# Performance work log

Measured on AMD Instinct MI355X. Metric: run time of the kernel, lower is better.

Reference implementation:

```python
import jax, jax.numpy as jnp
import numpy as np
import math

B = 262144
STATE = 6
TOTAL_MEAS = 27
HID = 256
INPUT_DIM = TOTAL_MEAS * 2 + 1 + STATE + 12  # 73
PI = math.pi
NORM_R_SCALE = 500.0 / 150000.0
ANG_IDX = np.array([0, 1, 3, 4, 6, 9, 10, 12, 13, 15, 18, 19, 21, 22, 24])
ANG_MASK = np.zeros((TOTAL_MEAS,), dtype=bool)
ANG_MASK[ANG_IDX] = True


def setup_inputs() -> dict:
    key = jax.random.key(0)
    ks = jax.random.split(key, 16)
    s = lambda fan: 1.0 / math.sqrt(fan)
    inp = {
        "meas": jax.random.normal(ks[0], (B, TOTAL_MEAS), jnp.float32),
        "mask": jnp.ones((B, TOTAL_MEAS), jnp.float32),
        "dt": jax.random.uniform(ks[1], (B,), jnp.float32),
        "baselines": jax.random.normal(ks[2], (B, 12), jnp.float32),
        "x_prev": jax.random.normal(ks[3], (B, STATE), jnp.float32),
        "hx": jnp.zeros((B, HID), jnp.float32),
        # GRU params (torch gate order: r, z, n)
        "W_ih": jax.random.uniform(ks[4], (3 * HID, INPUT_DIM), jnp.float32, -s(HID), s(HID)),
        "W_hh": jax.random.uniform(ks[5], (3 * HID, HID), jnp.float32, -s(HID), s(HID)),
        "b_ih": jax.random.uniform(ks[6], (3 * HID,), jnp.float32, -s(HID), s(HID)),
        "b_hh": jax.random.uniform(ks[7], (3 * HID,), jnp.float32, -s(HID), s(HID)),
        # LayerNorm
        "ln_g": jnp.ones((HID,), jnp.float32),
        "ln_b": jnp.zeros((HID,), jnp.float32),
        # MLP head: 256 -> 256 -> 128 -> 6*27
        "W1": jax.random.uniform(ks[8], (256, HID), jnp.float32, -s(HID), s(HID)),
        "b1": jax.random.uniform(ks[9], (256,), jnp.float32, -s(HID), s(HID)),
        "W2": jax.random.uniform(ks[10], (128, 256), jnp.float32, -s(256), s(256)),
        "b2": jax.random.uniform(ks[11], (128,), jnp.float32, -s(256), s(256)),
        "W3": jax.random.uniform(ks[12], (STATE * TOTAL_MEAS, 128), jnp.float32, -s(128), s(128)),
        "b3": jax.random.uniform(ks[13], (STATE * TOTAL_MEAS,), jnp.float32, -s(128), s(128)),
    }
    return inp


def _wrap_angle(a):
    two_pi = 2.0 * PI
    return a - two_pi * jnp.round(a / two_pi)


def _platform_y_pred(x_rel):
    # x_rel: [B, 6] -> [B, 9] radar/EO measurement
    r_xy = jnp.sqrt(x_rel[:, 0] ** 2 + x_rel[:, 2] ** 2 + 1e-9)
    az = jnp.arctan2(x_rel[:, 2], x_rel[:, 0]) / PI
    el = jnp.arctan2(x_rel[:, 4], r_xy) / PI
    r = jnp.sqrt(x_rel[:, 0] ** 2 + x_rel[:, 2] ** 2 + x_rel[:, 4] ** 2 + 1e-9)
    z = jnp.zeros_like(r)
    return jnp.stack([az, el, r, az, el, z, az, z, z], axis=1)


def _forward(meas, mask, dt, baselines, x_prev, hx,
             W_ih, W_hh, b_ih, b_hh, ln_g, ln_b, W1, b1, W2, b2, W3, b3):
    # f_predict (CV model): x0 += dt*x1, x2 += dt*x3, x4 += dt*x5
    dt_scaled = dt * NORM_R_SCALE  # [B]
    zcol = jnp.zeros_like(x_prev[:, :1])
    shift = jnp.concatenate([x_prev[:, 1:2], zcol, x_prev[:, 3:4], zcol, x_prev[:, 5:6], zcol], axis=1)
    x_minus = x_prev + dt_scaled[:, None] * shift  # [B, 6]

    y_pred = jnp.concatenate([
        _platform_y_pred(x_minus),
        _platform_y_pred(x_minus - baselines[:, 0:6]),
        _platform_y_pred(x_minus - baselines[:, 6:12]),
    ], axis=1)  # [B, 27]

    innov = meas - y_pred
    wrapped = _wrap_angle(innov * PI) / PI
    innov = jnp.where(jnp.asarray(ANG_MASK)[None, :], wrapped, innov)
    innov = innov * mask

    rnn_in = jnp.concatenate([innov, mask, dt[:, None], x_minus, baselines], axis=1)  # [B, 73]

    # single-step GRU (torch semantics, gate order r,z,n)
    gi = rnn_in @ W_ih.T + b_ih  # [B, 3H]
    gh = hx @ W_hh.T + b_hh      # [B, 3H]
    gi_r, gi_z, gi_n = jnp.split(gi, 3, axis=1)
    gh_r, gh_z, gh_n = jnp.split(gh, 3, axis=1)
    r = jax.nn.sigmoid(gi_r + gh_r)
    z = jax.nn.sigmoid(gi_z + gh_z)
    n = jnp.tanh(gi_n + r * gh_n)
    h_new = (1.0 - z) * n + z * hx  # [B, H]

    # LayerNorm
    mu = jnp.mean(h_new, axis=-1, keepdims=True)
    var = jnp.var(h_new, axis=-1, keepdims=True)
    h_ln = (h_new - mu) / jnp.sqrt(var + 1e-5) * ln_g + ln_b

    # MLP gain head (dropout inactive at inference)
    f1 = jax.nn.relu(h_ln @ W1.T + b1)
    f2 = jax.nn.relu(f1 @ W2.T + b2)
    K = (f2 @ W3.T + b3).reshape(-1, STATE, TOTAL_MEAS)
    K = jnp.clip(K, -3.0, 3.0)

    correction = jnp.einsum('bsm,bm->bs', K, innov)
    x_new = jnp.clip(x_minus + correction, -5.0, 5.0)
    return x_new, h_new


def reference(meas, mask, dt, baselines, x_prev, hx,
              W_ih, W_hh, b_ih, b_hh, ln_g, ln_b, W1, b1, W2, b2, W3, b3):
    return _forward(meas, mask, dt, baselines, x_prev, hx,
                    W_ih, W_hh, b_ih, b_hh, ln_g, ln_b, W1, b1, W2, b2, W3, b3)
```

## Files before the change

kernel.cpp:

```cpp
#include <hip/hip_runtime.h>
#include <math.h>

#define B_TOTAL  262144
#define ROWS     64
#define NWG      (B_TOTAL/ROWS)
#define NTHR     512
#define PI_F     3.14159265358979323846f
#define NORM_R   (500.0f/150000.0f)

typedef float  f32x4  __attribute__((ext_vector_type(4)));
typedef short  bf16x8 __attribute__((ext_vector_type(8)));

#define SRZ 352
#define SNI 96
#define SNH 256
#define SW1 256
#define SW2 256
#define SW3 128
#define OFF_RZ 0
#define OFF_NI (OFF_RZ + 512*SRZ)
#define OFF_NH (OFF_NI + 256*SNI)
#define OFF_W1 (OFF_NH + 256*SNH)
#define OFF_W2 (OFF_W1 + 256*SW1)
#define OFF_W3 (OFF_W2 + 128*SW2)
#define W_TOTAL (OFF_W3 + 256*SW3)

#define RSTRIDE 104
#define LDS_HB   (ROWS*RSTRIDE*2)
#define LDS_F1   (LDS_HB + ROWS*256*2)
#define LDS_STG  (LDS_F1 + ROWS*256*2)
#define LDS_XMC  (LDS_STG + 2*16384)
#define LDS_TOTAL (LDS_XMC + ROWS*6*4)

#define WAIT_VM2 asm volatile("s_waitcnt vmcnt(2)" ::: "memory")
#define WAIT_VM0 asm volatile("s_waitcnt vmcnt(0)" ::: "memory")
#define BARv     __builtin_amdgcn_s_barrier()

__device__ __forceinline__ ushort f2bf(float f){
    union { float f; unsigned u; } v; v.f = f;
    unsigned r = v.u + 0x7FFFu + ((v.u >> 16) & 1u);
    return (ushort)(r >> 16);
}
__device__ __forceinline__ float b2f(ushort u){
    union { unsigned u; float f; } v; v.u = ((unsigned)u) << 16;
    return v.f;
}
__device__ __forceinline__ float sigm(float x){ return 1.0f/(1.0f+__expf(-x)); }
__device__ __forceinline__ float tanh_(float x){ return 1.0f - 2.0f/(__expf(2.0f*x)+1.0f); }
__device__ __forceinline__ int swzb(int row, int k){
    return ((row<<9) + (k<<1)) ^ ((row&7)<<4);
}

__device__ __forceinline__ void stageA(const ushort* pb, int stride, int koff,
                                       char* dst, int w, int lane) {
    #pragma unroll
    for (int i = 0; i < 2; ++i) {
        int idx  = (w*2 + i)*64 + lane;
        int col  = idx >> 2;
        int kq   = (idx & 3) ^ ((col >> 1) & 3);
        const ushort* g = pb + (size_t)col*stride + koff + kq*8;
        __builtin_amdgcn_global_load_lds(
            (const __attribute__((address_space(1))) void*)g,
            (__attribute__((address_space(3))) void*)(dst + (w*2+i)*1024),
            16, 0, 0);
    }
}
__device__ __forceinline__ void stageB(const ushort* pb, int stride, int koff,
                                       char* dst, int w, int lane) {
    #pragma unroll
    for (int i = 0; i < 2; ++i) {
        int idx  = (w*2 + i)*64 + lane;
        int col  = idx >> 3;
        int kq   = (idx & 7) ^ (col & 7);
        const ushort* g = pb + (size_t)col*stride + koff + kq*8;
        __builtin_amdgcn_global_load_lds(
            (const __attribute__((address_space(1))) void*)g,
            (__attribute__((address_space(3))) void*)(dst + (w*2+i)*1024),
            16, 0, 0);
    }
}
__device__ __forceinline__ bf16x8 rdA16(const char* sb, int col, int lk){
    int slot = lk ^ ((col >> 1) & 3);
    return *(const bf16x8*)(sb + col*64 + slot*16);
}
__device__ __forceinline__ bf16x8 rdB16(const char* sb, int col, int ksub, int lk){
    int slot = ((ksub<<2)|lk) ^ (col & 7);
    return *(const bf16x8*)(sb + col*128 + slot*16);
}

__global__ void prep_weights(const float* __restrict__ W_ih, const float* __restrict__ W_hh,
                             const float* __restrict__ W1, const float* __restrict__ W2,
                             const float* __restrict__ W3, ushort* __restrict__ ws)
{
    int id = blockIdx.x*256 + threadIdx.x;
    if (id >= W_TOTAL) return;
    float v = 0.0f;
    if (id < OFF_NI) {
        int t = id; int n = t / SRZ, k = t - n*SRZ;
        if (k < 73) v = W_ih[n*73 + k];
        else if (k >= 96) v = W_hh[n*256 + (k-96)];
    } else if (id < OFF_NH) {
        int t = id - OFF_NI; int n = t / SNI, k = t - n*SNI;
        if (k < 73) v = W_ih[(512+n)*73 + k];
    } else if (id < OFF_W1) {
        int t = id - OFF_NH; int n = t >> 8, k = t & 255;
        v = W_hh[(512+n)*256 + k];
    } else if (id < OFF_W2) {
        int t = id - OFF_W1; int n = t >> 8, k = t & 255;
        v = W1[n*256 + k];
    } else if (id < OFF_W3) {
        int t = id - OFF_W2; int n = t >> 8, k = t & 255;
        v = W2[n*256 + k];
    } else {
        int t = id - OFF_W3; int n = t >> 7, k = t & 127;
        if (n < 162) v = W3[n*128 + k];
    }
    ws[id] = f2bf(v);
}

__global__ __launch_bounds__(NTHR, 2) void knet_mfma(
    const float* __restrict__ meas, const float* __restrict__ mask,
    const float* __restrict__ dt,   const float* __restrict__ baselines,
    const float* __restrict__ x_prev, const float* __restrict__ hx,
    const float* __restrict__ b_ih, const float* __restrict__ b_hh,
    const float* __restrict__ ln_g, const float* __restrict__ ln_b,
    const float* __restrict__ b1,   const float* __restrict__ b2,
    const float* __restrict__ b3,
    const ushort* __restrict__ ws,
    float* __restrict__ out)
{
    extern __shared__ char smem[];
    ushort* Rb  = (ushort*)smem;
    char*   Hb  = smem + LDS_HB;
    char*   F1  = smem + LDS_F1;
    char*   STG = smem + LDS_STG;
    float*  xmc = (float*)(smem + LDS_XMC);

    const int tid  = threadIdx.x;
    const int w    = __builtin_amdgcn_readfirstlane(tid >> 6);
    const int nq   = w & 3;
    const int mh   = w >> 2;
    const int lane = tid & 63;
    const int lr   = lane & 15;
    const int lk   = lane >> 4;
    const int lk8  = lk * 8;
    const int row0 = blockIdx.x * ROWS;
    const int mrow = mh*32 + lr;
    float* hout = out + (size_t)B_TOTAL*6;

    stageA(ws + OFF_RZ, SRZ, 0, STG, w, lane);

    {
        const int part = w;
        const int row  = lane;
        const int gb   = row0 + row;
        if (part < 4) {
            const float dtv = dt[gb];
            const float dts = dtv * NORM_R;
            float xp[6], xm[6];
            #pragma unroll
            for (int s = 0; s < 6; ++s) xp[s] = x_prev[(size_t)gb*6 + s];
            xm[0] = xp[0] + dts*xp[1]; xm[1] = xp[1];
            xm[2] = xp[2] + dts*xp[3]; xm[3] = xp[3];
            xm[4] = xp[4] + dts*xp[5]; xm[5] = xp[5];
            if (part < 3) {
                float xr[6];
                #pragma unroll
                for (int s = 0; s < 6; ++s) {
                    float b = (part == 0) ? 0.0f : baselines[(size_t)gb*12 + (part-1)*6 + s];
                    xr[s] = xm[s] - b;
                }
                float rxy = sqrtf(xr[0]*xr[0] + xr[2]*xr[2] + 1e-9f);
                float azv = atan2f(xr[2], xr[0]) * (1.0f/PI_F);
                float elv = atan2f(xr[4], rxy)   * (1.0f/PI_F);
                float rrv = sqrtf(xr[0]*xr[0] + xr[2]*xr[2] + xr[4]*xr[4] + 1e-9f);
                float y[9] = {azv, elv, rrv, azv, elv, 0.0f, azv, 0.0f, 0.0f};
                const bool ang[9] = {true,true,false,true,true,false,true,false,false};
                #pragma unroll
                for (int i = 0; i < 9; ++i) {
                    int m = part*9 + i;
                    float ms = mask[(size_t)gb*27 + m];
                    float v  = meas[(size_t)gb*27 + m] - y[i];
                    if (ang[i]) v = v - 2.0f*rintf(v*0.5f);
                    v *= ms;
                    Rb[row*RSTRIDE + m]      = f2bf(v);
                    Rb[row*RSTRIDE + 27 + m] = f2bf(ms);
                }
            } else {
                Rb[row*RSTRIDE + 54] = f2bf(dtv);
                #pragma unroll
                for (int s = 0; s < 6; ++s) Rb[row*RSTRIDE + 55 + s] = f2bf(xm[s]);
                #pragma unroll
                for (int q = 0; q < 12; ++q) Rb[row*RSTRIDE + 61 + q] = f2bf(baselines[(size_t)gb*12 + q]);
                #pragma unroll
                for (int k = 73; k < 96; ++k) Rb[row*RSTRIDE + k] = 0;
                #pragma unroll
                for (int s = 0; s < 6; ++s) xmc[row*6 + s] = xm[s];
            }
        }
        const size_t hbase = (size_t)row0 * 256;
        #pragma unroll
        for (int ii = 0; ii < 4; ++ii) {
            int cid = tid + ii*NTHR;
            int r  = cid >> 5;
            int k0 = (cid & 31) << 3;
            const float4* p = (const float4*)(hx + hbase + (size_t)r*256 + k0);
            float4 u = p[0], v2 = p[1];
            bf16x8 o;
            o[0]=(short)f2bf(u.x);  o[1]=(short)f2bf(u.y);  o[2]=(short)f2bf(u.z);  o[3]=(short)f2bf(u.w);
            o[4]=(short)f2bf(v2.x); o[5]=(short)f2bf(v2.y); o[6]=(short)f2bf(v2.z); o[7]=(short)f2bf(v2.w);
            *(bf16x8*)(Hb + swzb(r, k0)) = o;
        }
    }
    __syncthreads();

    f32x4 ar[2][4], az_[2][4], gi[2][4], gh[2][4];
    #pragma unroll
    for (int i = 0; i < 2; ++i)
        #pragma unroll
        for (int j = 0; j < 4; ++j) {
            ar[i][j]=(f32x4){0,0,0,0}; az_[i][j]=(f32x4){0,0,0,0};
            gi[i][j]=(f32x4){0,0,0,0}; gh[i][j]=(f32x4){0,0,0,0};
        }

    for (int kb = 0; kb < 11; ++kb) {
        char* nb = STG + (((kb+1)&1)<<14);
        if (kb < 10) stageA(ws + OFF_RZ, SRZ, (kb+1)*32, nb, w, lane);
        else         stageA(ws + OFF_RZ + (size_t)256*SRZ, SRZ, 0, nb, w, lane);
        WAIT_VM2; BARv;
        char* sb = STG + ((kb&1)<<14);
        bf16x8 a0, a1;
        if (kb < 3) { a0 = *(const bf16x8*)(Rb + mrow*RSTRIDE + kb*32 + lk8);
                      a1 = *(const bf16x8*)(Rb + (mrow+16)*RSTRIDE + kb*32 + lk8); }
        else        { a0 = *(const bf16x8*)(Hb + swzb(mrow,    (kb-3)*32 + lk8));
                      a1 = *(const bf16x8*)(Hb + swzb(mrow+16, (kb-3)*32 + lk8)); }
        __builtin_amdgcn_s_setprio(1);
        #pragma unroll
        for (int j = 0; j < 4; ++j) {
            bf16x8 b = rdA16(sb, nq*64 + j*16 + lr, lk);
            ar[0][j] = __builtin_amdgcn_mfma_f32_16x16x32_bf16(a0, b, ar[0][j], 0,0,0);
            ar[1][j] = __builtin_amdgcn_mfma_f32_16x16x32_bf16(a1, b, ar[1][j], 0,0,0);
        }
        __builtin_amdgcn_s_setprio(0);
        BARv;
    }
    for (int kb = 0; kb < 11; ++kb) {
        char* nb = STG + (((kb)&1)<<14);
        if (kb < 10) stageA(ws + OFF_RZ + (size_t)256*SRZ, SRZ, (kb+1)*32, nb, w, lane);
        else         stageA(ws + OFF_NI, SNI, 0, nb, w, lane);
        WAIT_VM2; BARv;
        char* sb = STG + (((kb+1)&1)<<14);
        bf16x8 a0, a1;
        if (kb < 3) { a0 = *(const bf16x8*)(Rb + mrow*RSTRIDE + kb*32 + lk8);
                      a1 = *(const bf16x8*)(Rb + (mrow+16)*RSTRIDE + kb*32 + lk8); }
        else        { a0 = *(const bf16x8*)(Hb + swzb(mrow,    (kb-3)*32 + lk8));
                      a1 = *(const bf16x8*)(Hb + swzb(mrow+16, (kb-3)*32 + lk8)); }
        __builtin_amdgcn_s_setprio(1);
        #pragma unroll
        for (int j = 0; j < 4; ++j) {
            bf16x8 b = rdA16(sb, nq*64 + j*16 + lr, lk);
            az_[0][j] = __builtin_amdgcn_mfma_f32_16x16x32_bf16(a0, b, az_[0][j], 0,0,0);
            az_[1][j] = __builtin_amdgcn_mfma_f32_16x16x32_bf16(a1, b, az_[1][j], 0,0,0);
        }
        __builtin_amdgcn_s_setprio(0);
        BARv;
    }
    for (int s = 0; s < 11; ++s) {
        char* nb = STG + (((s+23)&1)<<14);
        if (s < 2)       stageA(ws + OFF_NI, SNI, (s+1)*32, nb, w, lane);
        else if (s < 10) stageA(ws + OFF_NH, SNH, (s-2)*32, nb, w, lane);
        else             stageA(ws + OFF_W1, SW1, 0,        nb, w, lane);
        WAIT_VM2; BARv;
        char* sb = STG + (((s+22)&1)<<14);
        bf16x8 a0, a1;
        if (s < 3) { a0 = *(const bf16x8*)(Rb + mrow*RSTRIDE + s*32 + lk8);
                     a1 = *(const bf16x8*)(Rb + (mrow+16)*RSTRIDE + s*32 + lk8); }
        else       { a0 = *(const bf16x8*)(Hb + swzb(mrow,    (s-3)*32 + lk8));
                     a1 = *(const bf16x8*)(Hb + swzb(mrow+16, (s-3)*32 + lk8)); }
        __builtin_amdgcn_s_setprio(1);
        if (s < 3) {
            #pragma unroll
            for (int j = 0; j < 4; ++j) {
                bf16x8 b = rdA16(sb, nq*64 + j*16 + lr, lk);
                gi[0][j] = __builtin_amdgcn_mfma_f32_16x16x32_bf16(a0, b, gi[0][j], 0,0,0);
                gi[1][j] = __builtin_amdgcn_mfma_f32_16x16x32_bf16(a1, b, gi[1][j], 0,0,0);
            }
        } else {
            #pragma unroll
            for (int j = 0; j < 4; ++j) {
                bf16x8 b = rdA16(sb, nq*64 + j*16 + lr, lk);
                gh[0][j] = __builtin_amdgcn_mfma_f32_16x16x32_bf16(a0, b, gh[0][j], 0,0,0);
                gh[1][j] = __builtin_amdgcn_mfma_f32_16x16x32_bf16(a1, b, gh[1][j], 0,0,0);
            }
        }
        __builtin_amdgcn_s_setprio(0);
        BARv;
    }
    #pragma unroll
    for (int j = 0; j < 4; ++j) {
        int c = nq*64 + j*16 + lr;
        float brv = b_ih[c] + b_hh[c];
        float bzv = b_ih[256+c] + b_hh[256+c];
        float binv = b_ih[512+c], bhnv = b_hh[512+c];
        #pragma unroll
        for (int i = 0; i < 2; ++i)
            #pragma unroll
            for (int e = 0; e < 4; ++e) {
                int row = mh*32 + i*16 + lk*4 + e;
                float rg = sigm(ar[i][j][e] + brv);
                float zg = sigm(az_[i][j][e] + bzv);
                float ng = tanh_(gi[i][j][e] + binv + rg*(gh[i][j][e] + bhnv));
                float hxv = b2f(*(const ushort*)(Hb + swzb(row, c)));
                float hn = (1.0f - zg)*ng + zg*hxv;
                *(ushort*)(F1 + swzb(row, c)) = f2bf(hn);
            }
    }
    __syncthreads();

    {
        const int row = tid >> 3;
        const int o   = tid & 7;
        bf16x8 ch[4];
        float sum = 0.0f, sq = 0.0f;
        #pragma unroll
        for (int c4 = 0; c4 < 4; ++c4) {
            ch[c4] = *(const bf16x8*)(F1 + swzb(row, o*32 + c4*8));
            #pragma unroll
            for (int e = 0; e < 8; ++e) {
                float f = b2f((ushort)ch[c4][e]);
                sum += f; sq += f*f;
            }
        }
        sum += __shfl_xor(sum, 1); sum += __shfl_xor(sum, 2); sum += __shfl_xor(sum, 4);
        sq  += __shfl_xor(sq, 1);  sq  += __shfl_xor(sq, 2);  sq  += __shfl_xor(sq, 4);
        float mu   = sum * (1.0f/256.0f);
        float rstd = rsqrtf(sq*(1.0f/256.0f) - mu*mu + 1e-5f);
        #pragma unroll
        for (int c4 = 0; c4 < 4; ++c4) {
            int col0 = o*32 + c4*8;
            float4 g0 = *(const float4*)(ln_g + col0), g1 = *(const float4*)(ln_g + col0 + 4);
            float4 bb0 = *(const float4*)(ln_b + col0), bb1 = *(const float4*)(ln_b + col0 + 4);
            bf16x8 oo;
            oo[0] = (short)f2bf((b2f((ushort)ch[c4][0]) - mu)*rstd*g0.x + bb0.x);
            oo[1] = (short)f2bf((b2f((ushort)ch[c4][1]) - mu)*rstd*g0.y + bb0.y);
            oo[2] = (short)f2bf((b2f((ushort)ch[c4][2]) - mu)*rstd*g0.z + bb0.z);
            oo[3] = (short)f2bf((b2f((ushort)ch[c4][3]) - mu)*rstd*g0.w + bb0.w);
            oo[4] = (short)f2bf((b2f((ushort)ch[c4][4]) - mu)*rstd*g1.x + bb1.x);
            oo[5] = (short)f2bf((b2f((ushort)ch[c4][5]) - mu)*rstd*g1.y + bb1.y);
            oo[6] = (short)f2bf((b2f((ushort)ch[c4][6]) - mu)*rstd*g1.z + bb1.z);
            oo[7] = (short)f2bf((b2f((ushort)ch[c4][7]) - mu)*rstd*g1.w + bb1.w);
            *(bf16x8*)(Hb + swzb(row, col0)) = oo;
        }
        #pragma unroll
        for (int i = 0; i < 8; ++i) {
            int chunk = i*NTHR + tid;
            int r2 = chunk >> 6;
            int c16 = chunk & 63;
            uint2 d = *(const uint2*)(F1 + swzb(r2, c16*4));
            float4 o4;
            o4.x = b2f((ushort)(d.x & 0xffffu)); o4.y = b2f((ushort)(d.x >> 16));
            o4.z = b2f((ushort)(d.y & 0xffffu)); o4.w = b2f((ushort)(d.y >> 16));
            *(float4*)(hout + (size_t)(row0+r2)*256 + c16*4) = o4;
        }
    }
    __syncthreads();

    {
        f32x4 c2[2][4];
        #pragma unroll
        for (int i = 0; i < 2; ++i)
            #pragma unroll
            for (int j = 0; j < 4; ++j) c2[i][j] = (f32x4){0,0,0,0};
        for (int kb = 0; kb < 8; ++kb) {
            char* nb = STG + (((kb+34)&1)<<14);
            if (kb < 7) stageA(ws + OFF_W1, SW1, (kb+1)*32, nb, w, lane);
            else        stageB(ws + OFF_W2, SW2, 0,         nb, w, lane);
            WAIT_VM2; BARv;
            char* sb = STG + (((kb+33)&1)<<14);
            bf16x8 a0 = *(const bf16x8*)(Hb + swzb(mrow,    kb*32 + lk8));
            bf16x8 a1 = *(const bf16x8*)(Hb + swzb(mrow+16, kb*32 + lk8));
            __builtin_amdgcn_s_setprio(1);
            #pragma unroll
            for (int j = 0; j < 4; ++j) {
                bf16x8 b = rdA16(sb, nq*64 + j*16 + lr, lk);
                c2[0][j] = __builtin_amdgcn_mfma_f32_16x16x32_bf16(a0, b, c2[0][j], 0,0,0);
                c2[1][j] = __builtin_amdgcn_mfma_f32_16x16x32_bf16(a1, b, c2[1][j], 0,0,0);
            }
            __builtin_amdgcn_s_setprio(0);
            BARv;
        }
        #pragma unroll
        for (int j = 0; j < 4; ++j) {
            int c = nq*64 + j*16 + lr;
            float bv = b1[c];
            #pragma unroll
            for (int i = 0; i < 2; ++i)
                #pragma unroll
                for (int e = 0; e < 4; ++e) {
                    int row = mh*32 + i*16 + lk*4 + e;
                    *(ushort*)(F1 + swzb(row, c)) = f2bf(fmaxf(c2[i][j][e] + bv, 0.0f));
                }
        }
    }
    __syncthreads();

    ushort* F2 = (ushort*)Hb;
    {
        f32x4 c3[2][2];
        #pragma unroll
        for (int i = 0; i < 2; ++i)
            #pragma unroll
            for (int j = 0; j < 2; ++j) c3[i][j] = (f32x4){0,0,0,0};
        for (int kb = 0; kb < 4; ++kb) {
            char* nb = STG + (((kb+42)&1)<<14);
            if (kb < 3) stageB(ws + OFF_W2, SW2, (kb+1)*64, nb, w, lane);
            else        stageA(ws + OFF_W3, SW3, 0,         nb, w, lane);
            WAIT_VM2; BARv;
            char* sb = STG + (((kb+41)&1)<<14);
            __builtin_amdgcn_s_setprio(1);
            #pragma unroll
            for (int ksub = 0; ksub < 2; ++ksub) {
                bf16x8 a0 = *(const bf16x8*)(F1 + swzb(mrow,    kb*64 + ksub*32 + lk8));
                bf16x8 a1 = *(const bf16x8*)(F1 + swzb(mrow+16, kb*64 + ksub*32 + lk8));
                #pragma unroll
                for (int j = 0; j < 2; ++j) {
                    bf16x8 b = rdB16(sb, nq*32 + j*16 + lr, ksub, lk);
                    c3[0][j] = __builtin_amdgcn_mfma_f32_16x16x32_bf16(a0, b, c3[0][j], 0,0,0);
                    c3[1][j] = __builtin_amdgcn_mfma_f32_16x16x32_bf16(a1, b, c3[1][j], 0,0,0);
                }
            }
            __builtin_amdgcn_s_setprio(0);
            BARv;
        }
        __syncthreads();
        #pragma unroll
        for (int j = 0; j < 2; ++j) {
            int c = nq*32 + j*16 + lr;
            float bv = b2[c];
            #pragma unroll
            for (int i = 0; i < 2; ++i)
                #pragma unroll
                for (int e = 0; e < 4; ++e) {
                    int row = mh*32 + i*16 + lk*4 + e;
                    F2[row*136 + c] = f2bf(fmaxf(c3[i][j][e] + bv, 0.0f));
                }
        }
    }
    __syncthreads();

    {
        f32x4 c4[2][3];
        #pragma unroll
        for (int i = 0; i < 2; ++i)
            #pragma unroll
            for (int j = 0; j < 3; ++j) c4[i][j] = (f32x4){0,0,0,0};
        const int nfb = nq*3;
        for (int kb = 0; kb < 4; ++kb) {
            char* nb = STG + (((kb+46)&1)<<14);
            if (kb < 3) { stageA(ws + OFF_W3, SW3, (kb+1)*32, nb, w, lane); WAIT_VM2; }
            else        { WAIT_VM0; }
            BARv;
            char* sb = STG + (((kb+45)&1)<<14);
            bf16x8 a0 = *(const bf16x8*)(F2 + (mrow     )*136 + kb*32 + lk8);
            bf16x8 a1 = *(const bf16x8*)(F2 + (mrow + 16)*136 + kb*32 + lk8);
            __builtin_amdgcn_s_setprio(1);
            #pragma unroll
            for (int j = 0; j < 3; ++j) {
                bf16x8 b = rdA16(sb, (nfb+j)*16 + lr, lk);
                c4[0][j] = __builtin_amdgcn_mfma_f32_16x16x32_bf16(a0, b, c4[0][j], 0,0,0);
                c4[1][j] = __builtin_amdgcn_mfma_f32_16x16x32_bf16(a1, b, c4[1][j], 0,0,0);
            }
            __builtin_amdgcn_s_setprio(0);
            BARv;
        }
        #pragma unroll
        for (int j = 0; j < 3; ++j) {
            int col = (nfb+j)*16 + lr;
            if (col < 162) {
                int s = col / 27, m = col - s*27;
                float bv = b3[col];
                #pragma unroll
                for (int i = 0; i < 2; ++i)
                    #pragma unroll
                    for (int e = 0; e < 4; ++e) {
                        int row = mh*32 + i*16 + lk*4 + e;
                        float K  = fminf(fmaxf(c4[i][j][e] + bv, -3.0f), 3.0f);
                        float iv = b2f(Rb[row*RSTRIDE + m]);
                        atomicAdd(&xmc[row*6 + s], K*iv);
                    }
            }
        }
    }
    __syncthreads();

    for (int t = tid; t < ROWS*6; t += NTHR) {
        int row = t / 6, s = t - row*6;
        float v = fminf(fmaxf(xmc[t], -5.0f), 5.0f);
        out[(size_t)(row0+row)*6 + s] = v;
    }
}

extern "C" void kernel_launch(void* const* d_in, const int* in_sizes, int n_in,
                              void* d_out, int out_size, void* d_ws, size_t ws_size,
                              hipStream_t stream) {
    const float* meas      = (const float*)d_in[0];
    const float* mask      = (const float*)d_in[1];
    const float* dtv       = (const float*)d_in[2];
    const float* baselines = (const float*)d_in[3];
    const float* x_prev    = (const float*)d_in[4];
    const float* hx        = (const float*)d_in[5];
    const float* W_ih      = (const float*)d_in[6];
    const float* W_hh      = (const float*)d_in[7];
    const float* b_ih      = (const float*)d_in[8];
    const float* b_hh      = (const float*)d_in[9];
    const float* ln_g      = (const float*)d_in[10];
    const float* ln_b      = (const float*)d_in[11];
    const float* W1        = (const float*)d_in[12];
    const float* b1        = (const float*)d_in[13];
    const float* W2        = (const float*)d_in[14];
    const float* b2        = (const float*)d_in[15];
    const float* W3        = (const float*)d_in[16];
    const float* b3        = (const float*)d_in[17];
    ushort* wsb = (ushort*)d_ws;
    float* outp = (float*)d_out;

    prep_weights<<<(W_TOTAL + 255)/256, 256, 0, stream>>>(W_ih, W_hh, W1, W2, W3, wsb);
    knet_mfma<<<NWG, NTHR, LDS_TOTAL, stream>>>(
        meas, mask, dtv, baselines, x_prev, hx,
        b_ih, b_hh, ln_g, ln_b, b1, b2, b3, wsb, outp);
}
```

Baseline: 833.3 us.

## Deepen weight staging to 4-buffer ring with 3-ahead prefetch and one barrier per slice

Replaces the double-buffered weight staging with a four-slot ring that prefetches three K-slices ahead, using a unified slice index across all GEMM phases. This removes the trailing barrier per iteration and lets weight loads overlap more compute. Input rows (meas, mask, baselines, x_prev, dt) are now loaded cooperatively into LDS scratch with coalesced accesses before the per-row preprocessing. The cost is 32 KB more LDS per workgroup, which may reduce occupancy, plus an extra block-wide sync.

```diff
diff --git a/kernel.cpp b/kernel.cpp
--- a/kernel.cpp
+++ b/kernel.cpp
@@ -29,12 +29,14 @@
 #define LDS_HB   (ROWS*RSTRIDE*2)
 #define LDS_F1   (LDS_HB + ROWS*256*2)
 #define LDS_STG  (LDS_F1 + ROWS*256*2)
-#define LDS_XMC  (LDS_STG + 2*16384)
+#define LDS_XMC  (LDS_STG + 4*16384)
 #define LDS_TOTAL (LDS_XMC + ROWS*6*4)
 
+#define WAIT_VM4 asm volatile("s_waitcnt vmcnt(4)" ::: "memory")
 #define WAIT_VM2 asm volatile("s_waitcnt vmcnt(2)" ::: "memory")
 #define WAIT_VM0 asm volatile("s_waitcnt vmcnt(0)" ::: "memory")
 #define BARv     __builtin_amdgcn_s_barrier()
+#define N_SLICES 49
 
 __device__ __forceinline__ ushort f2bf(float f){
     union { float f; unsigned u; } v; v.f = f;
@@ -87,6 +89,32 @@
     int slot = ((ksub<<2)|lk) ^ (col & 7);
     return *(const bf16x8*)(sb + col*128 + slot*16);
 }
+
+__device__ __forceinline__ void stage_k(const ushort* ws, int k, char* STG, int w, int lane){
+    char* dst = STG + ((k & 3) << 14);
+    if (k < 11)      stageA(ws + OFF_RZ,                   SRZ, k*32,      dst, w, lane);
+    else if (k < 22) stageA(ws + OFF_RZ + (size_t)256*SRZ, SRZ, (k-11)*32, dst, w, lane);
+    else if (k < 25) stageA(ws + OFF_NI,                   SNI, (k-22)*32, dst, w, lane);
+    else if (k < 33) stageA(ws + OFF_NH,                   SNH, (k-25)*32, dst, w, lane);
+    else if (k < 41) stageA(ws + OFF_W1,                   SW1, (k-33)*32, dst, w, lane);
+    else if (k < 45) stageB(ws + OFF_W2,                   SW2, (k-41)*64, dst, w, lane);
+    else             stageA(ws + OFF_W3,                   SW3, (k-45)*32, dst, w, lane);
+}
+
+#define SLICE_PRE(kk) do { \
+    if ((kk) < N_SLICES-2)      WAIT_VM4; \
+    else if ((kk) == N_SLICES-2) WAIT_VM2; \
+    else                         WAIT_VM0; \
+    BARv; \
+    if ((kk)+3 < N_SLICES) stage_k(ws, (kk)+3, STG, w, lane); \
+} while(0)
+
+#define MM8(ACC) do { _Pragma("unroll") \
+    for (int j = 0; j < 4; ++j) { \
+        bf16x8 b = rdA16(sb, nq*64 + j*16 + lr, lk); \
+        ACC[0][j] = __builtin_amdgcn_mfma_f32_16x16x32_bf16(a0, b, ACC[0][j], 0,0,0); \
+        ACC[1][j] = __builtin_amdgcn_mfma_f32_16x16x32_bf16(a1, b, ACC[1][j], 0,0,0); \
+    } } while(0)
 
 __global__ void prep_weights(const float* __restrict__ W_ih, const float* __restrict__ W_hh,
                              const float* __restrict__ W1, const float* __restrict__ W2,
@@ -148,56 +176,19 @@
     const int mrow = mh*32 + lr;
     float* hout = out + (size_t)B_TOTAL*6;
 
-    stageA(ws + OFF_RZ, SRZ, 0, STG, w, lane);
-
+    stage_k(ws, 0, STG, w, lane);
+    stage_k(ws, 1, STG, w, lane);
+    stage_k(ws, 2, STG, w, lane);
+
+    float* scr = (float*)F1;
     {
-        const int part = w;
-        const int row  = lane;
-        const int gb   = row0 + row;
-        if (part < 4) {
-            const float dtv = dt[gb];
-            const float dts = dtv * NORM_R;
-            float xp[6], xm[6];
-            #pragma unroll
-            for (int s = 0; s < 6; ++s) xp[s] = x_prev[(size_t)gb*6 + s];
-            xm[0] = xp[0] + dts*xp[1]; xm[1] = xp[1];
-            xm[2] = xp[2] + dts*xp[3]; xm[3] = xp[3];
-            xm[4] = xp[4] + dts*xp[5]; xm[5] = xp[5];
-            if (part < 3) {
-                float xr[6];
-                #pragma unroll
-                for (int s = 0; s < 6; ++s) {
-                    float b = (part == 0) ? 0.0f : baselines[(size_t)gb*12 + (part-1)*6 + s];
-                    xr[s] = xm[s] - b;
-                }
-                float rxy = sqrtf(xr[0]*xr[0] + xr[2]*xr[2] + 1e-9f);
-                float azv = atan2f(xr[2], xr[0]) * (1.0f/PI_F);
-                float elv = atan2f(xr[4], rxy)   * (1.0f/PI_F);
-                float rrv = sqrtf(xr[0]*xr[0] + xr[2]*xr[2] + xr[4]*xr[4] + 1e-9f);
-                float y[9] = {azv, elv, rrv, azv, elv, 0.0f, azv, 0.0f, 0.0f};
-                const bool ang[9] = {true,true,false,true,true,false,true,false,false};
-                #pragma unroll
-                for (int i = 0; i < 9; ++i) {
-                    int m = part*9 + i;
-                    float ms = mask[(size_t)gb*27 + m];
-                    float v  = meas[(size_t)gb*27 + m] - y[i];
-                    if (ang[i]) v = v - 2.0f*rintf(v*0.5f);
-                    v *= ms;
-                    Rb[row*RSTRIDE + m]      = f2bf(v);
-                    Rb[row*RSTRIDE + 27 + m] = f2bf(ms);
-                }
-            } else {
-                Rb[row*RSTRIDE + 54] = f2bf(dtv);
-                #pragma unroll
-                for (int s = 0; s < 6; ++s) Rb[row*RSTRIDE + 55 + s] = f2bf(xm[s]);
-                #pragma unroll
-                for (int q = 0; q < 12; ++q) Rb[row*RSTRIDE + 61 + q] = f2bf(baselines[(size_t)gb*12 + q]);
-                #pragma unroll
-                for (int k = 73; k < 96; ++k) Rb[row*RSTRIDE + k] = 0;
-                #pragma unroll
-                for (int s = 0; s < 6; ++s) xmc[row*6 + s] = xm[s];
-            }
-        }
+        const size_t m0 = (size_t)row0*27;
+        for (int i = tid; i < 1728; i += NTHR) scr[i]        = meas[m0 + i];
+        for (int i = tid; i < 1728; i += NTHR) scr[1728 + i] = mask[m0 + i];
+        const size_t b0 = (size_t)row0*12;
+        for (int i = tid; i < 768; i += NTHR)  scr[3456 + i] = baselines[b0 + i];
+        if (tid < 384) scr[4224 + tid] = x_prev[(size_t)row0*6 + tid];
+        if (tid < 64)  scr[4608 + tid] = dt[row0 + tid];
         const size_t hbase = (size_t)row0 * 256;
         #pragma unroll
         for (int ii = 0; ii < 4; ++ii) {
@@ -214,6 +205,53 @@
     }
     __syncthreads();
 
+    if (w < 4) {
+        const int row = lane;
+        const float dtv = scr[4608 + row];
+        const float dts = dtv * NORM_R;
+        float xp[6], xm[6];
+        #pragma unroll
+        for (int s = 0; s < 6; ++s) xp[s] = scr[4224 + row*6 + s];
+        xm[0] = xp[0] + dts*xp[1]; xm[1] = xp[1];
+        xm[2] = xp[2] + dts*xp[3]; xm[3] = xp[3];
+        xm[4] = xp[4] + dts*xp[5]; xm[5] = xp[5];
+        if (w < 3) {
+            float xr[6];
+            #pragma unroll
+            for (int s = 0; s < 6; ++s) {
+                float b = (w == 0) ? 0.0f : scr[3456 + row*12 + (w-1)*6 + s];
+                xr[s] = xm[s] - b;
+            }
+            float rxy = sqrtf(xr[0]*xr[0] + xr[2]*xr[2] + 1e-9f);
+            float azv = atan2f(xr[2], xr[0]) * (1.0f/PI_F);
+            float elv = atan2f(xr[4], rxy)   * (1.0f/PI_F);
+            float rrv = sqrtf(xr[0]*xr[0] + xr[2]*xr[2] + xr[4]*xr[4] + 1e-9f);
+            float y[9] = {azv, elv, rrv, azv, elv, 0.0f, azv, 0.0f, 0.0f};
+            const bool ang[9] = {true,true,false,true,true,false,true,false,false};
+            #pragma unroll
+            for (int i = 0; i < 9; ++i) {
+                int m = w*9 + i;
+                float ms = scr[1728 + row*27 + m];
+                float v  = scr[row*27 + m] - y[i];
+                if (ang[i]) v = v - 2.0f*rintf(v*0.5f);
+                v *= ms;
+                Rb[row*RSTRIDE + m]      = f2bf(v);
+                Rb[row*RSTRIDE + 27 + m] = f2bf(ms);
+            }
+        } else {
+            Rb[row*RSTRIDE + 54] = f2bf(dtv);
+            #pragma unroll
+            for (int s = 0; s < 6; ++s) Rb[row*RSTRIDE + 55 + s] = f2bf(xm[s]);
+            #pragma unroll
+            for (int q = 0; q < 12; ++q) Rb[row*RSTRIDE + 61 + q] = f2bf(scr[3456 + row*12 + q]);
+            #pragma unroll
+            for (int k = 73; k < 96; ++k) Rb[row*RSTRIDE + k] = 0;
+            #pragma unroll
+            for (int s = 0; s < 6; ++s) xmc[row*6 + s] = xm[s];
+        }
+    }
+    __syncthreads();
+
     f32x4 ar[2][4], az_[2][4], gi[2][4], gh[2][4];
     #pragma unroll
     for (int i = 0; i < 2; ++i)
@@ -223,79 +261,27 @@
             gi[i][j]=(f32x4){0,0,0,0}; gh[i][j]=(f32x4){0,0,0,0};
         }
 
-    for (int kb = 0; kb < 11; ++kb) {
-        char* nb = STG + (((kb+1)&1)<<14);
-        if (kb < 10) stageA(ws + OFF_RZ, SRZ, (kb+1)*32, nb, w, lane);
-        else         stageA(ws + OFF_RZ + (size_t)256*SRZ, SRZ, 0, nb, w, lane);
-        WAIT_VM2; BARv;
-        char* sb = STG + ((kb&1)<<14);
+    int k = 0;
+    for (; k < 33; ++k) {
+        SLICE_PRE(k);
+        const char* sb = STG + ((k & 3) << 14);
         bf16x8 a0, a1;
-        if (kb < 3) { a0 = *(const bf16x8*)(Rb + mrow*RSTRIDE + kb*32 + lk8);
-                      a1 = *(const bf16x8*)(Rb + (mrow+16)*RSTRIDE + kb*32 + lk8); }
-        else        { a0 = *(const bf16x8*)(Hb + swzb(mrow,    (kb-3)*32 + lk8));
-                      a1 = *(const bf16x8*)(Hb + swzb(mrow+16, (kb-3)*32 + lk8)); }
+        if (k < 25) {
+            int kb = (k < 11) ? k : (k < 22) ? k-11 : k-22;
+            if (kb < 3) { a0 = *(const bf16x8*)(Rb + mrow*RSTRIDE + kb*32 + lk8);
+                          a1 = *(const bf16x8*)(Rb + (mrow+16)*RSTRIDE + kb*32 + lk8); }
+            else        { a0 = *(const bf16x8*)(Hb + swzb(mrow,    (kb-3)*32 + lk8));
+                          a1 = *(const bf16x8*)(Hb + swzb(mrow+16, (kb-3)*32 + lk8)); }
+        } else {
+            int hk = k - 25;
+            a0 = *(const bf16x8*)(Hb + swzb(mrow,    hk*32 + lk8));
+            a1 = *(const bf16x8*)(Hb + swzb(mrow+16, hk*32 + lk8));
+        }
         __builtin_amdgcn_s_setprio(1);
-        #pragma unroll
-        for (int j = 0; j < 4; ++j) {
-            bf16x8 b = rdA16(sb, nq*64 + j*16 + lr, lk);
-            ar[0][j] = __builtin_amdgcn_mfma_f32_16x16x32_bf16(a0, b, ar[0][j], 0,0,0);
-            ar[1][j] = __builtin_amdgcn_mfma_f32_16x16x32_bf16(a1, b, ar[1][j], 0,0,0);
-        }
+        if (k < 11) MM8(ar); else if (k < 22) MM8(az_); else if (k < 25) MM8(gi); else MM8(gh);
         __builtin_amdgcn_s_setprio(0);
-        BARv;
-    }
-    for (int kb = 0; kb < 11; ++kb) {
-        char* nb = STG + (((kb)&1)<<14);
-        if (kb < 10) stageA(ws + OFF_RZ + (size_t)256*SRZ, SRZ, (kb+1)*32, nb, w, lane);
-        else         stageA(ws + OFF_NI, SNI, 0, nb, w, lane);
-        WAIT_VM2; BARv;
-        char* sb = STG + (((kb+1)&1)<<14);
-        bf16x8 a0, a1;
-        if (kb < 3) { a0 = *(const bf16x8*)(Rb + mrow*RSTRIDE + kb*32 + lk8);
-                      a1 = *(const bf16x8*)(Rb + (mrow+16)*RSTRIDE + kb*32 + lk8); }
-        else        { a0 = *(const bf16x8*)(Hb + swzb(mrow,    (kb-3)*32 + lk8));
-                      a1 = *(const bf16x8*)(Hb + swzb(mrow+16, (kb-3)*32 + lk8)); }
-        __builtin_amdgcn_s_setprio(1);
-        #pragma unroll
-        for (int j = 0; j < 4; ++j) {
-            bf16x8 b = rdA16(sb, nq*64 + j*16 + lr, lk);
-            az_[0][j] = __builtin_amdgcn_mfma_f32_16x16x32_bf16(a0, b, az_[0][j], 0,0,0);
-            az_[1][j] = __builtin_amdgcn_mfma_f32_16x16x32_bf16(a1, b, az_[1][j], 0,0,0);
-        }
-        __builtin_amdgcn_s_setprio(0);
-        BARv;
-    }
-    for (int s = 0; s < 11; ++s) {
-        char* nb = STG + (((s+23)&1)<<14);
-        if (s < 2)       stageA(ws + OFF_NI, SNI, (s+1)*32, nb, w, lane);
-        else if (s < 10) stageA(ws + OFF_NH, SNH, (s-2)*32, nb, w, lane);
-        else             stageA(ws + OFF_W1, SW1, 0,        nb, w, lane);
-        WAIT_VM2; BARv;
-        char* sb = STG + (((s+22)&1)<<14);
-        bf16x8 a0, a1;
-        if (s < 3) { a0 = *(const bf16x8*)(Rb + mrow*RSTRIDE + s*32 + lk8);
-                     a1 = *(const bf16x8*)(Rb + (mrow+16)*RSTRIDE + s*32 + lk8); }
-        else       { a0 = *(const bf16x8*)(Hb + swzb(mrow,    (s-3)*32 + lk8));
-                     a1 = *(const bf16x8*)(Hb + swzb(mrow+16, (s-3)*32 + lk8)); }
-        __builtin_amdgcn_s_setprio(1);
-        if (s < 3) {
-            #pragma unroll
-            for (int j = 0; j < 4; ++j) {
-                bf16x8 b = rdA16(sb, nq*64 + j*16 + lr, lk);
-                gi[0][j] = __builtin_amdgcn_mfma_f32_16x16x32_bf16(a0, b, gi[0][j], 0,0,0);
-                gi[1][j] = __builtin_amdgcn_mfma_f32_16x16x32_bf16(a1, b, gi[1][j], 0,0,0);
-            }
-        } else {
-            #pragma unroll
-            for (int j = 0; j < 4; ++j) {
-                bf16x8 b = rdA16(sb, nq*64 + j*16 + lr, lk);
-                gh[0][j] = __builtin_amdgcn_mfma_f32_16x16x32_bf16(a0, b, gh[0][j], 0,0,0);
-                gh[1][j] = __builtin_amdgcn_mfma_f32_16x16x32_bf16(a1, b, gh[1][j], 0,0,0);
-            }
-        }
-        __builtin_amdgcn_s_setprio(0);
-        BARv;
-    }
+    }
+
     #pragma unroll
     for (int j = 0; j < 4; ++j) {
         int c = nq*64 + j*16 + lr;
@@ -371,24 +357,17 @@
         for (int i = 0; i < 2; ++i)
             #pragma unroll
             for (int j = 0; j < 4; ++j) c2[i][j] = (f32x4){0,0,0,0};
-        for (int kb = 0; kb < 8; ++kb) {
-            char* nb = STG + (((kb+34)&1)<<14);
-            if (kb < 7) stageA(ws + OFF_W1, SW1, (kb+1)*32, nb, w, lane);
-            else        stageB(ws + OFF_W2, SW2, 0,         nb, w, lane);
-            WAIT_VM2; BARv;
-            char* sb = STG + (((kb+33)&1)<<14);
+        for (; k < 41; ++k) {
+            SLICE_PRE(k);
+            const char* sb = STG + ((k & 3) << 14);
+            int kb = k - 33;
             bf16x8 a0 = *(const bf16x8*)(Hb + swzb(mrow,    kb*32 + lk8));
             bf16x8 a1 = *(const bf16x8*)(Hb + swzb(mrow+16, kb*32 + lk8));
             __builtin_amdgcn_s_setprio(1);
-            #pragma unroll
-            for (int j = 0; j < 4; ++j) {
-                bf16x8 b = rdA16(sb, nq*64 + j*16 + lr, lk);
-                c2[0][j] = __builtin_amdgcn_mfma_f32_16x16x32_bf16(a0, b, c2[0][j], 0,0,0);
-                c2[1][j] = __builtin_amdgcn_mfma_f32_16x16x32_bf16(a1, b, c2[1][j], 0,0,0);
-            }
+            MM8(c2);
             __builtin_amdgcn_s_setprio(0);
-            BARv;
-        }
+        }
+        __syncthreads();
         #pragma unroll
         for (int j = 0; j < 4; ++j) {
             int c = nq*64 + j*16 + lr;
@@ -411,12 +390,10 @@
         for (int i = 0; i < 2; ++i)
             #pragma unroll
             for (int j = 0; j < 2; ++j) c3[i][j] = (f32x4){0,0,0,0};
-        for (int kb = 0; kb < 4; ++kb) {
-            char* nb = STG + (((kb+42)&1)<<14);
-            if (kb < 3) stageB(ws + OFF_W2, SW2, (kb+1)*64, nb, w, lane);
-            else        stageA(ws + OFF_W3, SW3, 0,         nb, w, lane);
-            WAIT_VM2; BARv;
-            char* sb = STG + (((kb+41)&1)<<14);
+        for (; k < 45; ++k) {
+            SLICE_PRE(k);
+            const char* sb = STG + ((k & 3) << 14);
+            int kb = k - 41;
             __builtin_amdgcn_s_setprio(1);
             #pragma unroll
             for (int ksub = 0; ksub < 2; ++ksub) {
@@ -430,7 +407,6 @@
                 }
             }
             __builtin_amdgcn_s_setprio(0);
-            BARv;
         }
         __syncthreads();
         #pragma unroll
@@ -455,12 +431,10 @@
             #pragma unroll
             for (int j = 0; j < 3; ++j) c4[i][j] = (f32x4){0,0,0,0};
         const int nfb = nq*3;
-        for (int kb = 0; kb < 4; ++kb) {
-            char* nb = STG + (((kb+46)&1)<<14);
-            if (kb < 3) { stageA(ws + OFF_W3, SW3, (kb+1)*32, nb, w, lane); WAIT_VM2; }
-            else        { WAIT_VM0; }
-            BARv;
-            char* sb = STG + (((kb+45)&1)<<14);
+        for (; k < N_SLICES; ++k) {
+            SLICE_PRE(k);
+            const char* sb = STG + ((k & 3) << 14);
+            int kb = k - 45;
             bf16x8 a0 = *(const bf16x8*)(F2 + (mrow     )*136 + kb*32 + lk8);
             bf16x8 a1 = *(const bf16x8*)(F2 + (mrow + 16)*136 + kb*32 + lk8);
             __builtin_amdgcn_s_setprio(1);
@@ -471,7 +445,6 @@
                 c4[1][j] = __builtin_amdgcn_mfma_f32_16x16x32_bf16(a1, b, c4[1][j], 0,0,0);
             }
             __builtin_amdgcn_s_setprio(0);
-            BARv;
         }
         #pragma unroll
         for (int j = 0; j < 3; ++j) {
```

Result: slower. 1.104 ms (+32.4%).
